# Performance work log

Hardware: AMD Instinct MI355X
Metric: run time of the kernel (lower is better)

## Reference

```python
import jax, jax.numpy as jnp
import numpy as np

N_NODES = 65536
N_GRAPHS = 32
NODES_PER_GRAPH = 2048
N_EDGES = 1048576
F_IN, H1, H2, OUT = 16, 64, 64, 12


def gcn_conv(x, src, dst, W, b, num_nodes):
    """PyG GCNConv: out = D^{-1/2} (A+I) D^{-1/2} X W + b."""
    loop = jnp.arange(num_nodes, dtype=src.dtype)
    s = jnp.concatenate([src, loop])  # sources incl. self-loops
    d = jnp.concatenate([dst, loop])  # targets incl. self-loops
    deg = jax.ops.segment_sum(jnp.ones_like(d, dtype=x.dtype), d, num_segments=num_nodes)
    dinv = jnp.where(deg > 0, jax.lax.rsqrt(deg), 0.0)
    norm = dinv[s] * dinv[d]  # [E+N]
    h = x @ W  # [N, H]
    msg = h[s] * norm[:, None]  # [E+N, H] -- dominant memory traffic
    return jax.ops.segment_sum(msg, d, num_segments=num_nodes) + b


def setup_inputs() -> dict:
    key = jax.random.key(0)
    k = jax.random.split(key, 8)
    x = jax.random.normal(k[0], (N_NODES, F_IN), dtype=jnp.float32)
    edge_index = jax.random.randint(k[1], (2, N_EDGES), 0, N_NODES, dtype=jnp.int32)
    batch = jnp.repeat(jnp.arange(N_GRAPHS, dtype=jnp.int32), NODES_PER_GRAPH)
    s1 = 1.0 / np.sqrt(F_IN)
    s2 = 1.0 / np.sqrt(H1)
    s3 = 1.0 / np.sqrt(H2 * NODES_PER_GRAPH)
    W1 = jax.random.uniform(k[2], (F_IN, H1), jnp.float32, -s1, s1)
    b1 = jnp.zeros((H1,), jnp.float32)
    W2 = jax.random.uniform(k[3], (H1, H2), jnp.float32, -s2, s2)
    b2 = jnp.zeros((H2,), jnp.float32)
    Wfc = jax.random.uniform(k[4], (H2 * NODES_PER_GRAPH, OUT), jnp.float32, -s3, s3)
    bfc = jax.random.uniform(k[5], (OUT,), jnp.float32, -s3, s3)
    return {"x": x, "edge_index": edge_index, "batch": batch,
            "W1": W1, "b1": b1, "W2": W2, "b2": b2, "Wfc": Wfc, "bfc": bfc}


def reference(x, edge_index, batch, W1, b1, W2, b2, Wfc, bfc):
    src, dst = edge_index[0], edge_index[1]
    h = gcn_conv(x, src, dst, W1, b1, N_NODES)
    h = jnp.tanh(h)  # act1 (dropout rate 0 -> identity)
    h = gcn_conv(h, src, dst, W2, b2, N_NODES)
    h = jnp.tanh(h)  # act2
    # batch is sorted with exactly NODES_PER_GRAPH nodes per graph, so the
    # per-graph masked concat is a reshape: [G, P*H2]
    h_concat = h.reshape(N_GRAPHS, NODES_PER_GRAPH * H2)
    return h_concat @ Wfc + bfc
```

## Files before the change

### kernel.cpp

```cpp
#include <hip/hip_runtime.h>
#include <hip/hip_fp16.h>

#define N_NODES 65536
#define N_EDGES 1048576
#define F_IN    16
#define H       64
#define N_GRAPHS 32
#define NPG     2048
#define OUT_F   12
#define KPG     (NPG * H)
#define CAP     4864
#define NPB     16


__global__ __launch_bounds__(256) void init_kernel(int* __restrict__ gCursor,
                                                   const float* __restrict__ bfc,
                                                   float* __restrict__ out) {
    int t = threadIdx.x;
    gCursor[t] = t * CAP;
    for (int i = t; i < N_GRAPHS * OUT_F; i += 256) out[i] = bfc[i % OUT_F];
}

__global__ __launch_bounds__(256) void binA_kernel(const int* __restrict__ src,
                                                   const int* __restrict__ dst,
                                                   int* __restrict__ gCursor,
                                                   unsigned int* __restrict__ binned) {
    __shared__ int hist[256];
    __shared__ int sc[256];
    __shared__ int bnd[257];
    __shared__ int lcur[256];
    __shared__ int blkBase[256];
    __shared__ unsigned int staged[4096];
    int t = threadIdx.x;
    hist[t] = 0; lcur[t] = 0;
    __syncthreads();
    int e0 = blockIdx.x * 4096;
    unsigned int rec[16];
#pragma unroll
    for (int i = 0; i < 16; i++) {
        int e = e0 + i * 256 + t;
        unsigned int s = (unsigned int)src[e];
        unsigned int d = (unsigned int)dst[e];
        rec[i] = s | (d << 16);
        atomicAdd(&hist[d >> 8], 1);
    }
    __syncthreads();
    int cnt = hist[t];
    if (cnt) blkBase[t] = atomicAdd(&gCursor[t], cnt);
    sc[t] = cnt;
    __syncthreads();
    for (int off = 1; off < 256; off <<= 1) {
        int v = (t >= off) ? sc[t - off] : 0;
        __syncthreads();
        sc[t] += v;
        __syncthreads();
    }
    bnd[t] = sc[t] - cnt;
    if (t == 255) bnd[256] = 4096;
    __syncthreads();
#pragma unroll
    for (int i = 0; i < 16; i++) {
        int b = rec[i] >> 24;
        int p = bnd[b] + atomicAdd(&lcur[b], 1);
        staged[p] = rec[i];
    }
    __syncthreads();
    for (int i = t; i < 4096; i += 256) {
        int lo = 0;
#pragma unroll
        for (int s = 128; s > 0; s >>= 1)
            if (bnd[lo + s] <= i) lo += s;
        binned[blkBase[lo] + (i - bnd[lo])] = staged[i];
    }
}

__global__ __launch_bounds__(256) void binB_g1_kernel(const unsigned int* __restrict__ binned,
                                                      const int* __restrict__ gCursor,
                                                      const float* __restrict__ x,
                                                      int2* __restrict__ rowinfo,
                                                      unsigned short* __restrict__ nbr,
                                                      __half2* __restrict__ g1h) {
    __shared__ int hist[256];
    __shared__ int sc[256];
    __shared__ int off[256];
    __shared__ int cur[256];
    __shared__ unsigned short outS[8192];
    int b = blockIdx.x, t = threadIdx.x;
    int base = b * CAP;
    int cnt  = gCursor[b] - base;
    hist[t] = 0; cur[t] = 0;
    __syncthreads();
    for (int i = t; i < cnt; i += 256) {
        unsigned int r = binned[base + i];
        atomicAdd(&hist[(r >> 16) & 255], 1);
    }
    __syncthreads();
    int c = hist[t];
    sc[t] = c;
    __syncthreads();
    for (int o = 1; o < 256; o <<= 1) {
        int v = (t >= o) ? sc[t - o] : 0;
        __syncthreads();
        sc[t] += v;
        __syncthreads();
    }
    off[t] = sc[t] - c;
    int nd = (b << 8) + t;
    float dv = rsqrtf((float)(c + 1));
    rowinfo[nd] = make_int2(base + sc[t] - c, c);
    {
        const float4* xr = (const float4*)(x + (size_t)nd * F_IN);
        float4 x0 = xr[0], x1 = xr[1], x2 = xr[2], x3 = xr[3];
        __half2* gr = g1h + nd * 8;
        gr[0] = __floats2half2_rn(x0.x * dv, x0.y * dv);
        gr[1] = __floats2half2_rn(x0.z * dv, x0.w * dv);
        gr[2] = __floats2half2_rn(x1.x * dv, x1.y * dv);
        gr[3] = __floats2half2_rn(x1.z * dv, x1.w * dv);
        gr[4] = __floats2half2_rn(x2.x * dv, x2.y * dv);
        gr[5] = __floats2half2_rn(x2.z * dv, x2.w * dv);
        gr[6] = __floats2half2_rn(x3.x * dv, x3.y * dv);
        gr[7] = __floats2half2_rn(x3.z * dv, x3.w * dv);
    }
    __syncthreads();
    for (int i = t; i < cnt; i += 256) {
        unsigned int r = binned[base + i];
        int n = (r >> 16) & 255;
        int p = off[n] + atomicAdd(&cur[n], 1);
        outS[p] = (unsigned short)(r & 0xFFFF);
    }
    __syncthreads();
    for (int i = t; i < cnt; i += 256) nbr[base + i] = outS[i];
}

__device__ __forceinline__ void add8(float* acc, float4 q) {
    union { float4 f; __half2 h[4]; } u; u.f = q;
#pragma unroll
    for (int c = 0; c < 4; c++) {
        float2 p = __half22float2(u.h[c]);
        acc[2 * c]     += p.x;
        acc[2 * c + 1] += p.y;
    }
}
__device__ __forceinline__ void add4(float* acc, float2 q) {
    union { float2 f; __half2 h[2]; } u; u.f = q;
    float2 p0 = __half22float2(u.h[0]);
    float2 p1 = __half22float2(u.h[1]);
    acc[0] += p0.x; acc[1] += p0.y; acc[2] += p1.x; acc[3] += p1.y;
}

__global__ __launch_bounds__(256) void agg1_gemm1_kernel(const __half2* __restrict__ g1h,
                                                         const int2* __restrict__ rowinfo,
                                                         const unsigned short* __restrict__ nbr,
                                                         const float* __restrict__ W1,
                                                         const float* __restrict__ b1,
                                                         __half* __restrict__ g2h) {
    const float2* g1v = (const float2*)g1h;
    __shared__ float Ws[F_IN * H];
    __shared__ float bs[H];
    int t = threadIdx.x;
    for (int i = t; i < F_IN * H; i += 256) Ws[i] = W1[i];
    if (t < H) bs[t] = b1[t];
    __syncthreads();
    int lane = t & 63;
    int w    = t >> 6;
    int f4   = lane & 3;
    int sub  = lane >> 2;
    int v    = blockIdx.x * NPB + w;
    int2 ri  = rowinfo[v];
    int nb   = (int)nbr[ri.x + lane];
#pragma unroll 1
    for (int it = 0; it < NPB / 4; ++it) {
        int vc = v;
        int r0 = ri.x, er = ri.y;
        int nbc = nb;
        float2 sq = g1v[(vc << 2) + f4];
        if (it < NPB / 4 - 1) ri = rowinfo[vc + 4];
        float acc[4] = {0.f, 0.f, 0.f, 0.f};
        int j = 0;
        for (; j + 32 <= er; j += 32) {
            int u0 = __shfl(nbc, j + sub, 64);
            int u1 = __shfl(nbc, j + 16 + sub, 64);
            float2 q0 = g1v[(u0 << 2) + f4];
            float2 q1 = g1v[(u1 << 2) + f4];
            add4(acc, q0);
            add4(acc, q1);
        }
        for (; j < er && j < 64; j += 16) {
            int idx = j + sub;
            int u = __shfl(nbc, idx < er ? idx : 0, 64);
            float2 q = g1v[(u << 2) + f4];
            if (idx < er) add4(acc, q);
        }
        for (int base = 64; base < er; base += 64) {
            int nbx = (int)nbr[r0 + base + lane];
            for (int jj = 0; jj < 64 && base + jj < er; jj += 16) {
                int idx = jj + sub;
                int u = __shfl(nbx, (base + idx) < er ? idx : 0, 64);
                float2 q = g1v[(u << 2) + f4];
                if (base + idx < er) add4(acc, q);
            }
        }
        if (it < NPB / 4 - 1) nb = (int)nbr[ri.x + lane];
#pragma unroll
        for (int i = 0; i < 4; i++) {
            acc[i] += __shfl_xor(acc[i], 4, 64);
            acc[i] += __shfl_xor(acc[i], 8, 64);
            acc[i] += __shfl_xor(acc[i], 16, 64);
            acc[i] += __shfl_xor(acc[i], 32, 64);
        }
        add4(acc, sq);
        float dv = rsqrtf((float)(er + 1));
#pragma unroll
        for (int i = 0; i < 4; i++) acc[i] *= dv;
        float s = bs[lane];
#pragma unroll
        for (int k = 0; k < F_IN; ++k) {
            float bk = __shfl(acc[k & 3], k >> 2, 64);
            s += bk * Ws[k * H + lane];
        }
        g2h[(vc << 6) + lane] = __float2half(dv * tanhf(s));
        v += 4;
    }
}

__global__ __launch_bounds__(256) void agg2_kernel(const __half2* __restrict__ g2h,
                                                   const int2* __restrict__ rowinfo,
                                                   const unsigned short* __restrict__ nbr,
                                                   float* __restrict__ a2) {
    const float4* g2v = (const float4*)g2h;
    int t    = threadIdx.x;
    int lane = t & 63;
    int w    = t >> 6;
    int f8   = lane & 7;
    int sub  = lane >> 3;
    int v    = blockIdx.x * NPB + w;
    int2 ri  = rowinfo[v];
    int nb   = (int)nbr[ri.x + lane];
#pragma unroll 1
    for (int it = 0; it < NPB / 4; ++it) {
        int vc = v;
        int r0 = ri.x, er = ri.y;
        int nbc = nb;
        float4 sq = g2v[(vc << 3) + f8];
        if (it < NPB / 4 - 1) ri = rowinfo[vc + 4];
        float acc[8] = {0.f, 0.f, 0.f, 0.f, 0.f, 0.f, 0.f, 0.f};
        int j = 0;
        for (; j + 16 <= er; j += 16) {
            int u0 = __shfl(nbc, j + sub, 64);
            int u1 = __shfl(nbc, j + 8 + sub, 64);
            float4 q0 = g2v[(u0 << 3) + f8];
            float4 q1 = g2v[(u1 << 3) + f8];
            add8(acc, q0);
            add8(acc, q1);
        }
        for (; j < er && j < 64; j += 8) {
            int idx = j + sub;
            int u = __shfl(nbc, idx < er ? idx : 0, 64);
            float4 q = g2v[(u << 3) + f8];
            if (idx < er) add8(acc, q);
        }
        for (int base = 64; base < er; base += 64) {
            int nbx = (int)nbr[r0 + base + lane];
            for (int jj = 0; jj < 64 && base + jj < er; jj += 8) {
                int idx = jj + sub;
                int u = __shfl(nbx, (base + idx) < er ? idx : 0, 64);
                float4 q = g2v[(u << 3) + f8];
                if (base + idx < er) add8(acc, q);
            }
        }
        if (it < NPB / 4 - 1) nb = (int)nbr[ri.x + lane];
#pragma unroll
        for (int i = 0; i < 8; i++) {
            acc[i] += __shfl_xor(acc[i], 8, 64);
            acc[i] += __shfl_xor(acc[i], 16, 64);
            acc[i] += __shfl_xor(acc[i], 32, 64);
        }
        add8(acc, sq);
        float dv = rsqrtf((float)(er + 1));
#pragma unroll
        for (int i = 0; i < 8; i++) acc[i] *= dv;
        if (sub == 0) {
            float4* dp = (float4*)(a2 + ((size_t)vc << 6) + (f8 << 3));
            dp[0] = make_float4(acc[0], acc[1], acc[2], acc[3]);
            dp[1] = make_float4(acc[4], acc[5], acc[6], acc[7]);
        }
        v += 4;
    }
}

__global__ __launch_bounds__(256) void gemm2_fc_kernel(const float* __restrict__ a2,
                                                       const float* __restrict__ W2,
                                                       const float* __restrict__ b2,
                                                       const float* __restrict__ Wfc,
                                                       float* __restrict__ out) {
    __shared__ float Ws[H * H];
    __shared__ float As[64 * H];
    __shared__ float bs[H];
    __shared__ float red[4][OUT_F];
    int t = threadIdx.x;
    for (int i = t; i < H * H; i += 256) Ws[i] = W2[i];
    if (t < H) bs[t] = b2[t];
    {
        const float4* ap = (const float4*)(a2 + ((size_t)blockIdx.x << 12));
        float4* asp = (float4*)As;
#pragma unroll
        for (int i = 0; i < 4; i++) asp[i * 256 + t] = ap[i * 256 + t];
    }
    __syncthreads();
    int lane = t & 63, w = t >> 6;
    int v0 = blockIdx.x * 64 + (w << 4);
    int g  = blockIdx.x >> 5;
    float acc[16];
#pragma unroll
    for (int j = 0; j < 16; j++) acc[j] = bs[lane];
    const float* asBase = As + ((w << 4) * H);
#pragma unroll 2
    for (int kc = 0; kc < H / 4; ++kc) {
        int k0 = kc << 2;
        float w0 = Ws[(k0 + 0) * H + lane];
        float w1 = Ws[(k0 + 1) * H + lane];
        float w2 = Ws[(k0 + 2) * H + lane];
        float w3 = Ws[(k0 + 3) * H + lane];
#pragma unroll
        for (int j = 0; j < 16; ++j) {
            float4 aq = *(const float4*)(asBase + j * H + k0);
            acc[j] += aq.x * w0 + aq.y * w1 + aq.z * w2 + aq.w * w3;
        }
    }
    float pa[OUT_F];
#pragma unroll
    for (int j = 0; j < OUT_F; j++) pa[j] = 0.f;
#pragma unroll
    for (int j = 0; j < 16; ++j) {
        float hv = tanhf(acc[j]);
        int vl = (v0 + j) & (NPG - 1);
        const float4* wr = (const float4*)(Wfc + (size_t)(vl * H + lane) * OUT_F);
        float4 q0 = wr[0], q1 = wr[1], q2 = wr[2];
        pa[0]  += hv * q0.x;  pa[1]  += hv * q0.y;
        pa[2]  += hv * q0.z;  pa[3]  += hv * q0.w;
        pa[4]  += hv * q1.x;  pa[5]  += hv * q1.y;
        pa[6]  += hv * q1.z;  pa[7]  += hv * q1.w;
        pa[8]  += hv * q2.x;  pa[9]  += hv * q2.y;
        pa[10] += hv * q2.z;  pa[11] += hv * q2.w;
    }
#pragma unroll
    for (int j = 0; j < OUT_F; j++) {
        float vv = pa[j];
        vv += __shfl_xor(vv, 1, 64);  vv += __shfl_xor(vv, 2, 64);
        vv += __shfl_xor(vv, 4, 64);  vv += __shfl_xor(vv, 8, 64);
        vv += __shfl_xor(vv, 16, 64); vv += __shfl_xor(vv, 32, 64);
        pa[j] = vv;
    }
    if (lane == 0) {
#pragma unroll
        for (int j = 0; j < OUT_F; j++) red[w][j] = pa[j];
    }
    __syncthreads();
    if (t < OUT_F)
        atomicAdd(&out[g * OUT_F + t], red[0][t] + red[1][t] + red[2][t] + red[3][t]);
}

extern "C" void kernel_launch(void* const* d_in, const int* in_sizes, int n_in,
                              void* d_out, int out_size, void* d_ws, size_t ws_size,
                              hipStream_t stream) {
    const float* x    = (const float*)d_in[0];
    const int*   edge = (const int*)d_in[1];
    const int*   src  = edge;
    const int*   dst  = edge + N_EDGES;
    const float* W1  = (const float*)d_in[3];
    const float* b1  = (const float*)d_in[4];
    const float* W2  = (const float*)d_in[5];
    const float* b2  = (const float*)d_in[6];
    const float* Wfc = (const float*)d_in[7];
    const float* bfc = (const float*)d_in[8];
    float* out = (float*)d_out;

    char* p = (char*)d_ws;
    auto alloc = [&](size_t n) { char* r = p; p += (n + 255) & ~(size_t)255; return r; };
    int*   gCursor    = (int*)alloc(256 * 4);
    int2*  rowinfo    = (int2*)alloc((size_t)N_NODES * 8);
    unsigned short* nbr = (unsigned short*)alloc((size_t)256 * CAP * 2 + 256);
    __half* g1h       = (__half*)alloc((size_t)N_NODES * F_IN * 2);
    __half* g2h       = (__half*)alloc((size_t)N_NODES * H * 2);
    float* a2         = (float*)alloc((size_t)N_NODES * H * 4);
    unsigned int* binned = (unsigned int*)alloc((size_t)256 * CAP * 4);

    init_kernel<<<1, 256, 0, stream>>>(gCursor, bfc, out);
    binA_kernel<<<256, 256, 0, stream>>>(src, dst, gCursor, binned);
    binB_g1_kernel<<<256, 256, 0, stream>>>(binned, gCursor, x, rowinfo, nbr,
                                            (__half2*)g1h);
    agg1_gemm1_kernel<<<N_NODES / NPB, 256, 0, stream>>>((const __half2*)g1h, rowinfo, nbr,
                                                         W1, b1, g2h);
    agg2_kernel<<<N_NODES / NPB, 256, 0, stream>>>((const __half2*)g2h, rowinfo, nbr, a2);
    gemm2_fc_kernel<<<N_NODES / 64, 256, 0, stream>>>(a2, W2, b2, Wfc, out);
}
```

Measured before the change: 187.0 us.

## Remap FC blocks by position across graphs and prefetch first neighbor gathers

The final GEMM+FC kernel now gives each block two node positions across all 32 graphs instead of 64 consecutive nodes of one graph. The matching Wfc rows are loaded once into registers and reused for every graph, and the block writes 384 atomics instead of 12. Both aggregation kernels issue their first neighbor gathers with a guarded initial batch before the inner loop, so load latency overlaps with the row-info prefetch. The trade-off is a strided a2 gather, many more per-block atomics and shuffle reductions, and more registers.

```diff
diff --git a/kernel.cpp b/kernel.cpp
--- a/kernel.cpp
+++ b/kernel.cpp
@@ -174,16 +174,23 @@
         int r0 = ri.x, er = ri.y;
         int nbc = nb;
         float2 sq = g1v[(vc << 2) + f4];
+        int s0 = sub, s1 = 16 + sub;
+        int u0 = __shfl(nbc, s0 < er ? s0 : 0, 64);
+        int u1 = __shfl(nbc, s1 < er ? s1 : 0, 64);
+        float2 q0 = g1v[(u0 << 2) + f4];
+        float2 q1 = g1v[(u1 << 2) + f4];
         if (it < NPB / 4 - 1) ri = rowinfo[vc + 4];
         float acc[4] = {0.f, 0.f, 0.f, 0.f};
-        int j = 0;
+        if (s0 < er) add4(acc, q0);
+        if (s1 < er) add4(acc, q1);
+        int j = 32;
         for (; j + 32 <= er; j += 32) {
-            int u0 = __shfl(nbc, j + sub, 64);
-            int u1 = __shfl(nbc, j + 16 + sub, 64);
-            float2 q0 = g1v[(u0 << 2) + f4];
-            float2 q1 = g1v[(u1 << 2) + f4];
-            add4(acc, q0);
-            add4(acc, q1);
+            int a0 = __shfl(nbc, j + sub, 64);
+            int a1 = __shfl(nbc, j + 16 + sub, 64);
+            float2 t0 = g1v[(a0 << 2) + f4];
+            float2 t1 = g1v[(a1 << 2) + f4];
+            add4(acc, t0);
+            add4(acc, t1);
         }
         for (; j < er && j < 64; j += 16) {
             int idx = j + sub;
@@ -242,16 +249,29 @@
         int r0 = ri.x, er = ri.y;
         int nbc = nb;
         float4 sq = g2v[(vc << 3) + f8];
+        int s0 = sub, s1 = 8 + sub, s2 = 16 + sub, s3 = 24 + sub;
+        int u0 = __shfl(nbc, s0 < er ? s0 : 0, 64);
+        int u1 = __shfl(nbc, s1 < er ? s1 : 0, 64);
+        int u2 = __shfl(nbc, s2 < er ? s2 : 0, 64);
+        int u3 = __shfl(nbc, s3 < er ? s3 : 0, 64);
+        float4 q0 = g2v[(u0 << 3) + f8];
+        float4 q1 = g2v[(u1 << 3) + f8];
+        float4 q2 = g2v[(u2 << 3) + f8];
+        float4 q3 = g2v[(u3 << 3) + f8];
         if (it < NPB / 4 - 1) ri = rowinfo[vc + 4];
         float acc[8] = {0.f, 0.f, 0.f, 0.f, 0.f, 0.f, 0.f, 0.f};
-        int j = 0;
-        for (; j + 16 <= er; j += 16) {
-            int u0 = __shfl(nbc, j + sub, 64);
-            int u1 = __shfl(nbc, j + 8 + sub, 64);
-            float4 q0 = g2v[(u0 << 3) + f8];
-            float4 q1 = g2v[(u1 << 3) + f8];
-            add8(acc, q0);
-            add8(acc, q1);
+        if (s0 < er) add8(acc, q0);
+        if (s1 < er) add8(acc, q1);
+        if (s2 < er) add8(acc, q2);
+        if (s3 < er) add8(acc, q3);
+        int j = 32;
+        for (; j + 16 <= er && j < 64; j += 16) {
+            int a0 = __shfl(nbc, j + sub, 64);
+            int a1 = __shfl(nbc, j + 8 + sub, 64);
+            float4 t0 = g2v[(a0 << 3) + f8];
+            float4 t1 = g2v[(a1 << 3) + f8];
+            add8(acc, t0);
+            add8(acc, t1);
         }
         for (; j < er && j < 64; j += 8) {
             int idx = j + sub;
@@ -296,20 +316,31 @@
     __shared__ float Ws[H * H];
     __shared__ float As[64 * H];
     __shared__ float bs[H];
-    __shared__ float red[4][OUT_F];
+    __shared__ float red[N_GRAPHS * OUT_F];
     int t = threadIdx.x;
     for (int i = t; i < H * H; i += 256) Ws[i] = W2[i];
     if (t < H) bs[t] = b2[t];
+    int p0 = blockIdx.x << 1;
     {
-        const float4* ap = (const float4*)(a2 + ((size_t)blockIdx.x << 12));
+        const float4* a4 = (const float4*)a2;
         float4* asp = (float4*)As;
 #pragma unroll
-        for (int i = 0; i < 4; i++) asp[i * 256 + t] = ap[i * 256 + t];
-    }
-    __syncthreads();
+        for (int i = 0; i < 4; i++) {
+            int i4 = i * 256 + t;
+            int n = i4 >> 4, c = i4 & 15;
+            int g = n >> 1, q = n & 1;
+            asp[i4] = a4[(size_t)((g << 11) + p0 + q) * 16 + c];
+        }
+    }
     int lane = t & 63, w = t >> 6;
-    int v0 = blockIdx.x * 64 + (w << 4);
-    int g  = blockIdx.x >> 5;
+    float4 wf0a, wf0b, wf0c, wf1a, wf1b, wf1c;
+    {
+        const float4* wr0 = (const float4*)(Wfc + (size_t)(p0 * H + lane) * OUT_F);
+        const float4* wr1 = (const float4*)(Wfc + (size_t)((p0 + 1) * H + lane) * OUT_F);
+        wf0a = wr0[0]; wf0b = wr0[1]; wf0c = wr0[2];
+        wf1a = wr1[0]; wf1b = wr1[1]; wf1c = wr1[2];
+    }
+    __syncthreads();
     float acc[16];
 #pragma unroll
     for (int j = 0; j < 16; j++) acc[j] = bs[lane];
@@ -327,37 +358,33 @@
             acc[j] += aq.x * w0 + aq.y * w1 + aq.z * w2 + aq.w * w3;
         }
     }
-    float pa[OUT_F];
-#pragma unroll
-    for (int j = 0; j < OUT_F; j++) pa[j] = 0.f;
-#pragma unroll
-    for (int j = 0; j < 16; ++j) {
-        float hv = tanhf(acc[j]);
-        int vl = (v0 + j) & (NPG - 1);
-        const float4* wr = (const float4*)(Wfc + (size_t)(vl * H + lane) * OUT_F);
-        float4 q0 = wr[0], q1 = wr[1], q2 = wr[2];
-        pa[0]  += hv * q0.x;  pa[1]  += hv * q0.y;
-        pa[2]  += hv * q0.z;  pa[3]  += hv * q0.w;
-        pa[4]  += hv * q1.x;  pa[5]  += hv * q1.y;
-        pa[6]  += hv * q1.z;  pa[7]  += hv * q1.w;
-        pa[8]  += hv * q2.x;  pa[9]  += hv * q2.y;
-        pa[10] += hv * q2.z;  pa[11] += hv * q2.w;
-    }
-#pragma unroll
-    for (int j = 0; j < OUT_F; j++) {
-        float vv = pa[j];
-        vv += __shfl_xor(vv, 1, 64);  vv += __shfl_xor(vv, 2, 64);
-        vv += __shfl_xor(vv, 4, 64);  vv += __shfl_xor(vv, 8, 64);
-        vv += __shfl_xor(vv, 16, 64); vv += __shfl_xor(vv, 32, 64);
-        pa[j] = vv;
-    }
-    if (lane == 0) {
-#pragma unroll
-        for (int j = 0; j < OUT_F; j++) red[w][j] = pa[j];
-    }
-    __syncthreads();
-    if (t < OUT_F)
-        atomicAdd(&out[g * OUT_F + t], red[0][t] + red[1][t] + red[2][t] + red[3][t]);
+#pragma unroll
+    for (int gg = 0; gg < 8; ++gg) {
+        float h0 = tanhf(acc[2 * gg]);
+        float h1 = tanhf(acc[2 * gg + 1]);
+        float pa[OUT_F];
+        pa[0]  = h0 * wf0a.x + h1 * wf1a.x;  pa[1]  = h0 * wf0a.y + h1 * wf1a.y;
+        pa[2]  = h0 * wf0a.z + h1 * wf1a.z;  pa[3]  = h0 * wf0a.w + h1 * wf1a.w;
+        pa[4]  = h0 * wf0b.x + h1 * wf1b.x;  pa[5]  = h0 * wf0b.y + h1 * wf1b.y;
+        pa[6]  = h0 * wf0b.z + h1 * wf1b.z;  pa[7]  = h0 * wf0b.w + h1 * wf1b.w;
+        pa[8]  = h0 * wf0c.x + h1 * wf1c.x;  pa[9]  = h0 * wf0c.y + h1 * wf1c.y;
+        pa[10] = h0 * wf0c.z + h1 * wf1c.z;  pa[11] = h0 * wf0c.w + h1 * wf1c.w;
+#pragma unroll
+        for (int j = 0; j < OUT_F; j++) {
+            float vv = pa[j];
+            vv += __shfl_xor(vv, 1, 64);  vv += __shfl_xor(vv, 2, 64);
+            vv += __shfl_xor(vv, 4, 64);  vv += __shfl_xor(vv, 8, 64);
+            vv += __shfl_xor(vv, 16, 64); vv += __shfl_xor(vv, 32, 64);
+            pa[j] = vv;
+        }
+        if (lane == 0) {
+#pragma unroll
+            for (int j = 0; j < OUT_F; j++) red[(w * 8 + gg) * OUT_F + j] = pa[j];
+        }
+    }
+    __syncthreads();
+    for (int i = t; i < N_GRAPHS * OUT_F; i += 256)
+        atomicAdd(&out[i], red[i]);
 }
 
 extern "C" void kernel_launch(void* const* d_in, const int* in_sizes, int n_in,
@@ -392,5 +419,5 @@
     agg1_gemm1_kernel<<<N_NODES / NPB, 256, 0, stream>>>((const __half2*)g1h, rowinfo, nbr,
                                                          W1, b1, g2h);
     agg2_kernel<<<N_NODES / NPB, 256, 0, stream>>>((const __half2*)g2h, rowinfo, nbr, a2);
-    gemm2_fc_kernel<<<N_NODES / 64, 256, 0, stream>>>(a2, W2, b2, Wfc, out);
-}
+    gemm2_fc_kernel<<<NPG / 2, 256, 0, stream>>>(a2, W2, b2, Wfc, out);
+}
```

Result: slower. 206.8 us (+10.6%).
